# Kernel tuning notes

Hardware: AMD Instinct MI355X
Metric: run time of the kernel (lower is better)

The kernel has to match this reference:

```python
import jax, jax.numpy as jnp
import numpy as np

D_MODEL = 1024
NUM_HEADS = 16
D_K = D_MODEL // NUM_HEADS
LN_EPS = 1e-5


def setup_inputs() -> dict:
    key = jax.random.key(0)
    ks = jax.random.split(key, 16)
    B, SQ, SK = 2, 2048, 2048
    s = 1.0 / np.sqrt(D_MODEL)
    inp = {
        "query": jax.random.normal(ks[0], (B, SQ, D_MODEL), jnp.float32),
        "key": jax.random.normal(ks[1], (B, SK, D_MODEL), jnp.float32),
        "value": jax.random.normal(ks[2], (B, SK, D_MODEL), jnp.float32),
        "mask": jax.random.randint(ks[3], (B, SQ, SK), 0, 2, jnp.int32),
        "w_q": jax.random.normal(ks[4], (D_MODEL, D_MODEL), jnp.float32) * s,
        "b_q": jnp.zeros((D_MODEL,), jnp.float32),
        "w_k": jax.random.normal(ks[5], (D_MODEL, D_MODEL), jnp.float32) * s,
        "b_k": jnp.zeros((D_MODEL,), jnp.float32),
        "w_v": jax.random.normal(ks[6], (D_MODEL, D_MODEL), jnp.float32) * s,
        "b_v": jnp.zeros((D_MODEL,), jnp.float32),
        "w_o": jax.random.normal(ks[7], (D_MODEL, D_MODEL), jnp.float32) * s,
        "b_o": jnp.zeros((D_MODEL,), jnp.float32),
        "ln_gamma": jnp.ones((D_MODEL,), jnp.float32),
        "ln_beta": jnp.zeros((D_MODEL,), jnp.float32),
    }
    return inp


def _split_heads(x):
    B, S, _ = x.shape
    return x.reshape(B, S, NUM_HEADS, D_K).transpose(0, 2, 1, 3)  # [B,H,S,Dk]


def reference(query, key, value, mask, w_q, b_q, w_k, b_k, w_v, b_v, w_o, b_o, ln_gamma, ln_beta):
    residual = query
    # torch Linear: y = x @ W.T + b
    Q = _split_heads(jnp.einsum('bsd,ed->bse', query, w_q) + b_q)
    K = _split_heads(jnp.einsum('bsd,ed->bse', key, w_k) + b_k)
    V = _split_heads(jnp.einsum('bsd,ed->bse', value, w_v) + b_v)
    scores = jnp.einsum('bhqd,bhkd->bhqk', Q, K) / jnp.sqrt(jnp.float32(D_K))
    scores = jnp.where(mask[:, None, :, :] == 0, jnp.float32(-1e9), scores)
    attn = jax.nn.softmax(scores, axis=-1)
    # dropout: eval mode (identity)
    ctx = jnp.einsum('bhqk,bhkd->bhqd', attn, V)
    B, H, SQ, Dk = ctx.shape
    ctx = ctx.transpose(0, 2, 1, 3).reshape(B, SQ, D_MODEL)
    out = jnp.einsum('bsd,ed->bse', ctx, w_o) + b_o + residual
    mu = jnp.mean(out, axis=-1, keepdims=True)
    var = jnp.mean(jnp.square(out - mu), axis=-1, keepdims=True)
    out = (out - mu) * jax.lax.rsqrt(var + LN_EPS) * ln_gamma + ln_beta
    return out
```

## Files before the change

kernel.cpp:

```cpp
#include <hip/hip_runtime.h>

typedef unsigned short u16;
typedef __attribute__((ext_vector_type(8))) short bf16x8;
typedef __attribute__((ext_vector_type(4))) float f32x4;

#define LOG2E 1.4426950408889634f
#define QSCALE (LOG2E / 8.0f)

__device__ __forceinline__ u16 f2bf(float f) {
  union { float f; unsigned u; } v; v.f = f;
  unsigned r = v.u + 0x7fffu + ((v.u >> 16) & 1u);
  return (u16)(r >> 16);
}

__device__ __forceinline__ void gload_lds16(const void* g, void* l) {
  __builtin_amdgcn_global_load_lds(
      (const __attribute__((address_space(1))) unsigned int*)(unsigned long long)g,
      (__attribute__((address_space(3))) unsigned int*)(unsigned int)(unsigned long long)l,
      16, 0, 0);
}

__global__ __launch_bounds__(256) void prep_kernel(
    const float* __restrict__ q, const float* __restrict__ k, const float* __restrict__ v,
    const float* __restrict__ wq, const float* __restrict__ wk, const float* __restrict__ wv,
    const float* __restrict__ wo, const int* __restrict__ mask,
    u16* __restrict__ Xq, u16* __restrict__ Xk, u16* __restrict__ Xv,
    u16* __restrict__ Wq, u16* __restrict__ Wk, u16* __restrict__ Wv, u16* __restrict__ Wo,
    unsigned long long* __restrict__ Mp) {
  const int bx = blockIdx.x;
  if (bx < 16384) {
    const float* src; u16* dst; float sc; int idx;
    if (bx < 12288) {
      int seg = bx >> 12;
      idx = (bx & 4095) * 256 + threadIdx.x;
      src = seg == 0 ? q : (seg == 1 ? k : v);
      dst = seg == 0 ? Xq : (seg == 1 ? Xk : Xv);
      sc = 1.f;
    } else {
      int t = bx - 12288, seg = t >> 10;
      idx = (t & 1023) * 256 + threadIdx.x;
      src = seg == 0 ? wq : (seg == 1 ? wk : (seg == 2 ? wv : wo));
      dst = seg == 0 ? Wq : (seg == 1 ? Wk : (seg == 2 ? Wv : Wo));
      sc = seg == 0 ? QSCALE : 1.f;
    }
    float4 x = ((const float4*)src)[idx];
    ushort4 o;
    o.x = f2bf(x.x * sc); o.y = f2bf(x.y * sc);
    o.z = f2bf(x.z * sc); o.w = f2bf(x.w * sc);
    ((ushort4*)dst)[idx] = o;
  } else {
    int gw = (((bx - 16384) * 256) + threadIdx.x) >> 6;
    int lane = threadIdx.x & 63;
    for (int w = gw; w < 131072; w += 16384) {
      int m = mask[(size_t)w * 64 + lane];
      unsigned long long b = __ballot(m != 0);
      if (lane == 0) Mp[w] = b;
    }
  }
}

__global__ __launch_bounds__(256, 3) void gemm_kernel(
    const u16* __restrict__ Xq, const u16* __restrict__ Xk, const u16* __restrict__ Xv,
    const u16* __restrict__ Wq, const u16* __restrict__ Wk, const u16* __restrict__ Wv,
    const u16* __restrict__ Wo, const u16* __restrict__ Ctx,
    const float* __restrict__ bq, const float* __restrict__ bk, const float* __restrict__ bv,
    u16* __restrict__ Qd, u16* __restrict__ Kd, u16* __restrict__ Vtd, float* __restrict__ outp,
    int mode_base) {
  __shared__ __align__(16) u16 SH[17408];
  u16* As = SH;
  u16* Bs = SH + 4096;
  const int mode = mode_base + blockIdx.z;
  const int tid = threadIdx.x;
  const int wid = tid >> 6, l = tid & 63, quad = l >> 4, ln = l & 15;
  const int wm = wid >> 1, wn = wid & 1;

  const u16 *A, *B; const float* bias;
  if (mode == 0)      { A = Wq; B = Xq;  bias = bq; }
  else if (mode == 1) { A = Wk; B = Xk;  bias = bk; }
  else if (mode == 2) { A = Xv; B = Wv;  bias = bv; }
  else                { A = Wo; B = Ctx; bias = bq; }
  int mBase, nBase;
  if (mode == 2) { mBase = blockIdx.x * 128; nBase = blockIdx.y * 128; }
  else           { mBase = blockIdx.y * 128; nBase = blockIdx.x * 128; }

  const u16* Ag = A + (size_t)mBase * 1024;
  const u16* Bg = B + (size_t)nBase * 1024;

  f32x4 acc[4][4] = {};

  for (int k0 = 0; k0 < 1024; k0 += 32) {
    if (k0) __syncthreads();
    {
      int i0 = tid, i1 = tid + 256;
      gload_lds16(Ag + (size_t)(i0 & 127) * 1024 + k0 + (i0 >> 7) * 8, &As[i0 * 8]);
      gload_lds16(Ag + (size_t)(i1 & 127) * 1024 + k0 + (i1 >> 7) * 8, &As[i1 * 8]);
      gload_lds16(Bg + (size_t)(i0 & 127) * 1024 + k0 + (i0 >> 7) * 8, &Bs[i0 * 8]);
      gload_lds16(Bg + (size_t)(i1 & 127) * 1024 + k0 + (i1 >> 7) * 8, &Bs[i1 * 8]);
    }
    __syncthreads();
    bf16x8 af[4], bf[4];
#pragma unroll
    for (int i = 0; i < 4; ++i)
      af[i] = *(const bf16x8*)&As[(quad * 128 + wm * 64 + i * 16 + ln) * 8];
#pragma unroll
    for (int j = 0; j < 4; ++j)
      bf[j] = *(const bf16x8*)&Bs[(quad * 128 + wn * 64 + j * 16 + ln) * 8];
#pragma unroll
    for (int i = 0; i < 4; ++i)
#pragma unroll
      for (int j = 0; j < 4; ++j)
        acc[i][j] = __builtin_amdgcn_mfma_f32_16x16x32_bf16(af[i], bf[j], acc[i][j], 0, 0, 0);
  }

  __syncthreads();

  if (mode <= 1) {
    const float bscale = (mode == 0) ? QSCALE : 1.0f;
#pragma unroll
    for (int i = 0; i < 4; ++i) {
      int f0 = wm * 64 + i * 16 + quad * 4;
      float4 bb = *(const float4*)(bias + mBase + f0);
#pragma unroll
      for (int j = 0; j < 4; ++j) {
        int sl = wn * 64 + j * 16 + ln;
        f32x4 v = acc[i][j];
        ushort4 o;
        o.x = f2bf(v[0] + bb.x * bscale); o.y = f2bf(v[1] + bb.y * bscale);
        o.z = f2bf(v[2] + bb.z * bscale); o.w = f2bf(v[3] + bb.w * bscale);
        *(ushort4*)&SH[sl * 136 + f0] = o;
      }
    }
    __syncthreads();
    u16* dstQK = (mode == 0) ? Qd : Kd;
#pragma unroll
    for (int p = 0; p < 8; ++p) {
      int sl = p * 16 + (tid >> 4);
      int fl = (tid & 15) * 8;
      uint4 w = *(const uint4*)&SH[sl * 136 + fl];
      int s = nBase + sl, f = mBase + fl;
      int h = f >> 6, d = f & 63, b = s >> 11, sr = s & 2047;
      *(uint4*)(dstQK + (((size_t)(b * 16 + h) * 2048 + sr) * 64 + d)) = w;
    }
  } else if (mode == 2) {
#pragma unroll
    for (int j = 0; j < 4; ++j) {
      int fl = wn * 64 + j * 16 + ln;
      float bb = bias[nBase + fl];
#pragma unroll
      for (int i = 0; i < 4; ++i) {
        int s0 = wm * 64 + i * 16 + quad * 4;
        f32x4 v = acc[i][j];
        ushort4 o;
        o.x = f2bf(v[0] + bb); o.y = f2bf(v[1] + bb);
        o.z = f2bf(v[2] + bb); o.w = f2bf(v[3] + bb);
        *(ushort4*)&SH[fl * 136 + s0] = o;
      }
    }
    __syncthreads();
#pragma unroll
    for (int p = 0; p < 8; ++p) {
      int fl = p * 16 + (tid >> 4);
      int sl = (tid & 15) * 8;
      uint4 w = *(const uint4*)&SH[fl * 136 + sl];
      int f = nBase + fl, s = mBase + sl;
      int h = f >> 6, d = f & 63, b = s >> 11, sr = s & 2047;
      *(uint4*)(Vtd + (((size_t)(b * 16 + h) * 64 + d) * 2048 + sr)) = w;
    }
  } else {
    float* ES = (float*)SH;
#pragma unroll
    for (int h2 = 0; h2 < 2; ++h2) {
      if (h2) __syncthreads();
      if (wn == h2) {
#pragma unroll
        for (int i = 0; i < 4; ++i) {
          int f0 = wm * 64 + i * 16 + quad * 4;
#pragma unroll
          for (int j = 0; j < 4; ++j) {
            int sl = j * 16 + ln;
            f32x4 v = acc[i][j];
            float4 o; o.x = v[0]; o.y = v[1]; o.z = v[2]; o.w = v[3];
            *(float4*)&ES[sl * 132 + f0] = o;
          }
        }
      }
      __syncthreads();
#pragma unroll
      for (int p = 0; p < 8; ++p) {
        int sl = p * 8 + (tid >> 5);
        int fl = (tid & 31) * 4;
        float4 w = *(const float4*)&ES[sl * 132 + fl];
        int s = nBase + h2 * 64 + sl;
        *(float4*)(outp + (size_t)s * 1024 + mBase + fl) = w;
      }
    }
  }
}

__global__ __launch_bounds__(512, 4) void attn_kernel(
    const u16* __restrict__ Qg, const u16* __restrict__ Kg, const u16* __restrict__ Vtg,
    const unsigned* __restrict__ Mp, u16* __restrict__ ctx) {
  __shared__ __align__(16) u16 Ks0[8192];
  __shared__ __align__(16) u16 Ks1[8192];
  __shared__ __align__(16) u16 Vs0[8192];
  __shared__ __align__(16) u16 Vs1[8192];
  __shared__ __align__(16) u16 Ps[8192];
  const int tid = threadIdx.x;
  const int wid = tid >> 6, l = tid & 63, quad = l >> 4, ln = l & 15;
  const int q4 = quad * 4;
  const int L = blockIdx.x;
  const int bh = (L & 7) + 8 * (L >> 7);
  const int b = bh >> 4, h = bh & 15;
  const int qBase = ((L >> 3) & 15) * 128;
  const int wq = wid * 16;
  const int sw = (ln & 7) << 3;

  bf16x8 qf[2];
#pragma unroll
  for (int kc = 0; kc < 2; ++kc)
    qf[kc] = *(const bf16x8*)(Qg + (((size_t)bh * 2048 + qBase + wq + ln) * 64 +
                                    kc * 32 + quad * 8));

  f32x4 oacc[4] = {};
  f32x4 lsum = {};
  const bf16x8 vone = {(short)0x3F80, (short)0x3F80, (short)0x3F80, (short)0x3F80,
                       (short)0x3F80, (short)0x3F80, (short)0x3F80, (short)0x3F80};

  const unsigned* mrow = Mp + ((size_t)b * 2048 + qBase + wq + ln) * 64;

  const u16* KgB = Kg + (size_t)bh * 2048 * 64;
  const u16* VgB = Vtg + (size_t)bh * 64 * 2048;

#define STAGE_TILE(KS, VS, t_)                                                  \
  do {                                                                          \
    const int kvB_ = (t_) * 128;                                                \
    _Pragma("unroll")                                                           \
    for (int r_ = 0; r_ < 2; ++r_) {                                            \
      int c_ = r_ * 512 + tid;                                                  \
      gload_lds16(KgB + (size_t)(kvB_ + (c_ & 127)) * 64 + (c_ >> 7) * 8,       \
                  &KS[c_ * 8]);                                                 \
      gload_lds16(VgB + (size_t)(c_ & 63) * 2048 + kvB_ + (c_ >> 6) * 8,        \
                  &VS[c_ * 8]);                                                 \
    }                                                                           \
  } while (0)

#define COMPUTE_TILE(KS, VS, it_)                                                         \
  do {                                                                                    \
    unsigned ww[4];                                                                       \
    {                                                                                     \
      uint4 m0 = *(const uint4*)(mrow + (it_) * 4);                                       \
      ww[0] = m0.x; ww[1] = m0.y; ww[2] = m0.z; ww[3] = m0.w;                             \
    }                                                                                     \
    _Pragma("unroll")                                                                     \
    for (int hf = 0; hf < 2; ++hf) {                                                      \
      f32x4 s[4];                                                                         \
      __builtin_amdgcn_s_setprio(1);                                                      \
      _Pragma("unroll")                                                                   \
      for (int m2 = 0; m2 < 4; ++m2) {                                                    \
        int mt = hf * 4 + m2;                                                             \
        bf16x8 k0 = *(const bf16x8*)&KS[((0 + quad) * 128 + mt * 16 + ln) * 8];           \
        bf16x8 k1 = *(const bf16x8*)&KS[((4 + quad) * 128 + mt * 16 + ln) * 8];           \
        f32x4 z = {0.f, 0.f, 0.f, 0.f};                                                   \
        z = __builtin_amdgcn_mfma_f32_16x16x32_bf16(k0, qf[0], z, 0, 0, 0);               \
        s[m2] = __builtin_amdgcn_mfma_f32_16x16x32_bf16(k1, qf[1], z, 0, 0, 0);           \
      }                                                                                   \
      __builtin_amdgcn_s_setprio(0);                                                      \
      uint2 pk[4];                                                                        \
      _Pragma("unroll")                                                                   \
      for (int m2 = 0; m2 < 4; ++m2) {                                                    \
        int mt = hf * 4 + m2;                                                             \
        unsigned nib = (ww[mt >> 1] >> ((mt & 1) * 16 + q4)) & 0xFu;                      \
        float p0 = __builtin_amdgcn_exp2f((nib & 1u) ? s[m2][0] : -1e30f);                \
        float p1 = __builtin_amdgcn_exp2f((nib & 2u) ? s[m2][1] : -1e30f);                \
        float p2 = __builtin_amdgcn_exp2f((nib & 4u) ? s[m2][2] : -1e30f);                \
        float p3 = __builtin_amdgcn_exp2f((nib & 8u) ? s[m2][3] : -1e30f);                \
        pk[m2].x = __builtin_amdgcn_perm(__float_as_uint(p1), __float_as_uint(p0),        \
                                         0x07060302u);                                    \
        pk[m2].y = __builtin_amdgcn_perm(__float_as_uint(p3), __float_as_uint(p2),        \
                                         0x07060302u);                                    \
      }                                                                                   \
              \
      _Pragma("unroll")                                                                   \
      for (int m2 = 0; m2 < 4; ++m2)                                                      \
        *(uint2*)&Ps[(((wq + ln) * 64) + m2 * 16 + q4) ^ sw] = pk[m2];                    \
      __builtin_amdgcn_s_setprio(1);                                                      \
      _Pragma("unroll")                                                                   \
      for (int k2 = 0; k2 < 2; ++k2) {                                                    \
        int kc2 = hf * 2 + k2;                                                            \
        bf16x8 aP = *(const bf16x8*)&Ps[(((wq + ln) * 64) + k2 * 32 + quad * 8) ^ sw];    \
        _Pragma("unroll")                                                                 \
        for (int nt = 0; nt < 4; ++nt) {                                                  \
          bf16x8 bV = *(const bf16x8*)&VS[((kc2 * 4 + quad) * 64 + nt * 16 + ln) * 8];    \
          oacc[nt] = __builtin_amdgcn_mfma_f32_16x16x32_bf16(aP, bV, oacc[nt], 0, 0, 0);  \
        }                                                                                 \
        lsum = __builtin_amdgcn_mfma_f32_16x16x32_bf16(aP, vone, lsum, 0, 0, 0);          \
      }                                                                                   \
      __builtin_amdgcn_s_setprio(0);                                                      \
    }                                                                                     \
  } while (0)

  STAGE_TILE(Ks0, Vs0, 0);
#pragma unroll 1
  for (int it2 = 0; it2 < 8; ++it2) {
    __syncthreads();
    STAGE_TILE(Ks1, Vs1, 2 * it2 + 1);
    COMPUTE_TILE(Ks0, Vs0, 2 * it2);
    __syncthreads();
    if (it2 < 7) STAGE_TILE(Ks0, Vs0, 2 * it2 + 2);
    COMPUTE_TILE(Ks1, Vs1, 2 * it2 + 1);
  }
#undef STAGE_TILE
#undef COMPUTE_TILE

  __syncthreads();
#pragma unroll
  for (int r = 0; r < 4; ++r) {
    float il = 1.0f / lsum[r];
    int q = wq + q4 + r;
#pragma unroll
    for (int nt = 0; nt < 4; ++nt)
      Ps[q * 64 + nt * 16 + ln] = f2bf(oacc[nt][r] * il);
  }
  __syncthreads();
#pragma unroll
  for (int r = 0; r < 2; ++r) {
    int c = r * 512 + tid;
    int q = c >> 3, ch = c & 7;
    *(uint4*)(ctx + ((size_t)(b * 2048 + qBase + q) * 1024 + h * 64 + ch * 8)) =
        *(const uint4*)&Ps[q * 64 + ch * 8];
  }
}

__global__ __launch_bounds__(256) void ln_kernel(const float* __restrict__ x,
                                                 const float* __restrict__ resid,
                                                 const float* __restrict__ bo,
                                                 const float* __restrict__ gamma,
                                                 const float* __restrict__ beta,
                                                 float* __restrict__ out) {
  __shared__ float red[8];
  const int tid = threadIdx.x;
  const size_t row = blockIdx.x;
  float4 v = ((const float4*)(x + row * 1024))[tid];
  const float4 rr = ((const float4*)(resid + row * 1024))[tid];
  const float4 bb = ((const float4*)bo)[tid];
  v.x += rr.x + bb.x; v.y += rr.y + bb.y; v.z += rr.z + bb.z; v.w += rr.w + bb.w;
  float s1 = v.x + v.y + v.z + v.w;
  float s2 = v.x * v.x + v.y * v.y + v.z * v.z + v.w * v.w;
#pragma unroll
  for (int o = 32; o >= 1; o >>= 1) {
    s1 += __shfl_xor(s1, o);
    s2 += __shfl_xor(s2, o);
  }
  if ((tid & 63) == 0) { red[(tid >> 6) * 2] = s1; red[(tid >> 6) * 2 + 1] = s2; }
  __syncthreads();
  s1 = red[0] + red[2] + red[4] + red[6];
  s2 = red[1] + red[3] + red[5] + red[7];
  float mu = s1 * (1.f / 1024.f);
  float var = s2 * (1.f / 1024.f) - mu * mu;
  float inv = rsqrtf(var + 1e-5f);
  float4 g = ((const float4*)gamma)[tid];
  float4 be = ((const float4*)beta)[tid];
  float4 o;
  o.x = (v.x - mu) * inv * g.x + be.x;
  o.y = (v.y - mu) * inv * g.y + be.y;
  o.z = (v.z - mu) * inv * g.z + be.z;
  o.w = (v.w - mu) * inv * g.w + be.w;
  ((float4*)(out + row * 1024))[tid] = o;
}

extern "C" void kernel_launch(void* const* d_in, const int* in_sizes, int n_in,
                              void* d_out, int out_size, void* d_ws, size_t ws_size,
                              hipStream_t stream) {
  const float* query = (const float*)d_in[0];
  const float* key   = (const float*)d_in[1];
  const float* value = (const float*)d_in[2];
  const int*   mask  = (const int*)d_in[3];
  const float* w_q = (const float*)d_in[4];
  const float* b_q = (const float*)d_in[5];
  const float* w_k = (const float*)d_in[6];
  const float* b_k = (const float*)d_in[7];
  const float* w_v = (const float*)d_in[8];
  const float* b_v = (const float*)d_in[9];
  const float* w_o = (const float*)d_in[10];
  const float* b_o = (const float*)d_in[11];
  const float* ln_g = (const float*)d_in[12];
  const float* ln_b = (const float*)d_in[13];
  float* out = (float*)d_out;

  char* ws = (char*)d_ws;
  u16* Xq = (u16*)(ws + ((size_t)0 << 20));
  u16* Xk = (u16*)(ws + ((size_t)8 << 20));
  u16* Xv = (u16*)(ws + ((size_t)16 << 20));
  float* outpre = (float*)(ws + ((size_t)8 << 20));
  u16* Wq = (u16*)(ws + ((size_t)24 << 20));
  u16* Wk = (u16*)(ws + ((size_t)26 << 20));
  u16* Wv = (u16*)(ws + ((size_t)28 << 20));
  u16* Wo = (u16*)(ws + ((size_t)30 << 20));
  u16* Qd = (u16*)(ws + ((size_t)32 << 20));
  u16* Kd = (u16*)(ws + ((size_t)40 << 20));
  u16* Vtd = (u16*)(ws + ((size_t)48 << 20));
  unsigned long long* Mp = (unsigned long long*)(ws + ((size_t)56 << 20));
  u16* ctx = Xq;

  prep_kernel<<<20480, 256, 0, stream>>>(query, key, value, w_q, w_k, w_v, w_o, mask,
                                         Xq, Xk, Xv, Wq, Wk, Wv, Wo, Mp);
  gemm_kernel<<<dim3(32, 8, 3), 256, 0, stream>>>(Xq, Xk, Xv, Wq, Wk, Wv, Wo, ctx,
      b_q, b_k, b_v, Qd, Kd, Vtd, outpre, 0);
  attn_kernel<<<dim3(512), 512, 0, stream>>>(Qd, Kd, Vtd, (const unsigned*)Mp, ctx);
  gemm_kernel<<<dim3(32, 8, 1), 256, 0, stream>>>(Xq, Xk, Xv, Wq, Wk, Wv, Wo, ctx,
      b_q, b_k, b_v, Qd, Kd, Vtd, outpre, 3);
  ln_kernel<<<4096, 256, 0, stream>>>(outpre, query, b_o, ln_g, ln_b, out);
}
```

Baseline: 308.6 us.

## Split output projection GEMM along K into two bf16 partials summed in LayerNorm

The output projection GEMM launches twice as many blocks, each covering half of the K dimension, to fill more CUs than the previous 256-block grid. Each half writes a bf16 partial result instead of fp32, and the LayerNorm kernel reads and adds both partials along with the residual and bias. This adds parallelism and shrinks the intermediate write size. In exchange it loses precision, because the partials are rounded to bf16 before they are summed.

```diff
diff --git a/kernel.cpp b/kernel.cpp
--- a/kernel.cpp
+++ b/kernel.cpp
@@ -11,6 +11,10 @@
   union { float f; unsigned u; } v; v.f = f;
   unsigned r = v.u + 0x7fffu + ((v.u >> 16) & 1u);
   return (u16)(r >> 16);
+}
+
+__device__ __forceinline__ float bf2f(u16 u) {
+  union { unsigned u; float f; } v; v.u = (unsigned)u << 16; return v.f;
 }
 
 __device__ __forceinline__ void gload_lds16(const void* g, void* l) {
@@ -64,7 +68,7 @@
     const u16* __restrict__ Wq, const u16* __restrict__ Wk, const u16* __restrict__ Wv,
     const u16* __restrict__ Wo, const u16* __restrict__ Ctx,
     const float* __restrict__ bq, const float* __restrict__ bk, const float* __restrict__ bv,
-    u16* __restrict__ Qd, u16* __restrict__ Kd, u16* __restrict__ Vtd, float* __restrict__ outp,
+    u16* __restrict__ Qd, u16* __restrict__ Kd, u16* __restrict__ Vtd, u16* __restrict__ outp,
     int mode_base) {
   __shared__ __align__(16) u16 SH[17408];
   u16* As = SH;
@@ -83,12 +87,14 @@
   if (mode == 2) { mBase = blockIdx.x * 128; nBase = blockIdx.y * 128; }
   else           { mBase = blockIdx.y * 128; nBase = blockIdx.x * 128; }
 
-  const u16* Ag = A + (size_t)mBase * 1024;
-  const u16* Bg = B + (size_t)nBase * 1024;
+  const int koff = (mode >= 3) ? (mode - 3) * 512 : 0;
+  const int kLen = (mode >= 3) ? 512 : 1024;
+  const u16* Ag = A + (size_t)mBase * 1024 + koff;
+  const u16* Bg = B + (size_t)nBase * 1024 + koff;
 
   f32x4 acc[4][4] = {};
 
-  for (int k0 = 0; k0 < 1024; k0 += 32) {
+  for (int k0 = 0; k0 < kLen; k0 += 32) {
     if (k0) __syncthreads();
     {
       int i0 = tid, i1 = tid + 256;
@@ -167,32 +173,27 @@
       *(uint4*)(Vtd + (((size_t)(b * 16 + h) * 64 + d) * 2048 + sr)) = w;
     }
   } else {
-    float* ES = (float*)SH;
-#pragma unroll
-    for (int h2 = 0; h2 < 2; ++h2) {
-      if (h2) __syncthreads();
-      if (wn == h2) {
-#pragma unroll
-        for (int i = 0; i < 4; ++i) {
-          int f0 = wm * 64 + i * 16 + quad * 4;
-#pragma unroll
-          for (int j = 0; j < 4; ++j) {
-            int sl = j * 16 + ln;
-            f32x4 v = acc[i][j];
-            float4 o; o.x = v[0]; o.y = v[1]; o.z = v[2]; o.w = v[3];
-            *(float4*)&ES[sl * 132 + f0] = o;
-          }
-        }
+    u16* dst = outp + (size_t)(mode - 3) * (4096u * 1024u);
+#pragma unroll
+    for (int i = 0; i < 4; ++i) {
+      int f0 = wm * 64 + i * 16 + quad * 4;
+#pragma unroll
+      for (int j = 0; j < 4; ++j) {
+        int sl = wn * 64 + j * 16 + ln;
+        f32x4 v = acc[i][j];
+        ushort4 o;
+        o.x = f2bf(v[0]); o.y = f2bf(v[1]);
+        o.z = f2bf(v[2]); o.w = f2bf(v[3]);
+        *(ushort4*)&SH[sl * 136 + f0] = o;
       }
-      __syncthreads();
-#pragma unroll
-      for (int p = 0; p < 8; ++p) {
-        int sl = p * 8 + (tid >> 5);
-        int fl = (tid & 31) * 4;
-        float4 w = *(const float4*)&ES[sl * 132 + fl];
-        int s = nBase + h2 * 64 + sl;
-        *(float4*)(outp + (size_t)s * 1024 + mBase + fl) = w;
-      }
+    }
+    __syncthreads();
+#pragma unroll
+    for (int p = 0; p < 8; ++p) {
+      int sl = p * 16 + (tid >> 4);
+      int fl = (tid & 15) * 8;
+      uint4 w = *(const uint4*)&SH[sl * 136 + fl];
+      *(uint4*)(dst + (size_t)(nBase + sl) * 1024 + mBase + fl) = w;
     }
   }
 }
@@ -331,7 +332,7 @@
   }
 }
 
-__global__ __launch_bounds__(256) void ln_kernel(const float* __restrict__ x,
+__global__ __launch_bounds__(256) void ln_kernel(const u16* __restrict__ xp,
                                                  const float* __restrict__ resid,
                                                  const float* __restrict__ bo,
                                                  const float* __restrict__ gamma,
@@ -340,10 +341,15 @@
   __shared__ float red[8];
   const int tid = threadIdx.x;
   const size_t row = blockIdx.x;
-  float4 v = ((const float4*)(x + row * 1024))[tid];
+  ushort4 pa = ((const ushort4*)(xp + row * 1024))[tid];
+  ushort4 pb = ((const ushort4*)(xp + 4096u * 1024u + row * 1024))[tid];
   const float4 rr = ((const float4*)(resid + row * 1024))[tid];
   const float4 bb = ((const float4*)bo)[tid];
-  v.x += rr.x + bb.x; v.y += rr.y + bb.y; v.z += rr.z + bb.z; v.w += rr.w + bb.w;
+  float4 v;
+  v.x = bf2f(pa.x) + bf2f(pb.x) + rr.x + bb.x;
+  v.y = bf2f(pa.y) + bf2f(pb.y) + rr.y + bb.y;
+  v.z = bf2f(pa.z) + bf2f(pb.z) + rr.z + bb.z;
+  v.w = bf2f(pa.w) + bf2f(pb.w) + rr.w + bb.w;
   float s1 = v.x + v.y + v.z + v.w;
   float s2 = v.x * v.x + v.y * v.y + v.z * v.z + v.w * v.w;
 #pragma unroll
@@ -391,7 +397,7 @@
   u16* Xq = (u16*)(ws + ((size_t)0 << 20));
   u16* Xk = (u16*)(ws + ((size_t)8 << 20));
   u16* Xv = (u16*)(ws + ((size_t)16 << 20));
-  float* outpre = (float*)(ws + ((size_t)8 << 20));
+  u16* outpre = (u16*)(ws + ((size_t)8 << 20));
   u16* Wq = (u16*)(ws + ((size_t)24 << 20));
   u16* Wk = (u16*)(ws + ((size_t)26 << 20));
   u16* Wv = (u16*)(ws + ((size_t)28 << 20));
@@ -407,7 +413,7 @@
   gemm_kernel<<<dim3(32, 8, 3), 256, 0, stream>>>(Xq, Xk, Xv, Wq, Wk, Wv, Wo, ctx,
       b_q, b_k, b_v, Qd, Kd, Vtd, outpre, 0);
   attn_kernel<<<dim3(512), 512, 0, stream>>>(Qd, Kd, Vtd, (const unsigned*)Mp, ctx);
-  gemm_kernel<<<dim3(32, 8, 1), 256, 0, stream>>>(Xq, Xk, Xv, Wq, Wk, Wv, Wo, ctx,
+  gemm_kernel<<<dim3(32, 8, 2), 256, 0, stream>>>(Xq, Xk, Xv, Wq, Wk, Wv, Wo, ctx,
       b_q, b_k, b_v, Qd, Kd, Vtd, outpre, 3);
   ln_kernel<<<4096, 256, 0, stream>>>(outpre, query, b_o, ln_g, ln_b, out);
 }
```

Result: faster. 297.1 us, median of 2 (-3.7%).
